# Kernel tuning notes

Hardware: AMD Instinct MI355X
Metric: run time of the kernel (lower is better)

The kernel has to match this reference:

```python
import jax, jax.numpy as jnp
import numpy as np

L = 8          # context_length
P = 196        # patches_per_frame
PT = 16        # patches_per_tactile_frame
N_EMBD = 768
N_HEAD = 12
BATCH = 4
T = (L + 1) + L * PT + L * P  # 1705


def build_mask(L, P, Pt):
    # image-query block rows (L*P rows)
    mi = np.zeros((L * P, L * P))
    a1 = np.zeros((L * P, L + 1))
    t1 = np.zeros((L * P, L * Pt))
    for i in range(L):
        mi[i * P:(i + 1) * P, :(i + 1) * P] = 1
        a1[i * P:(i + 2) * P, :i + 2] = 1
        t1[i * P:(i + 1) * P, :(i + 1) * Pt] = 1
    m1 = np.concatenate([a1, t1, mi], axis=1)
    # tactile-query block rows (L*Pt rows)
    a2 = np.zeros((L * Pt, L + 1))
    t2 = np.zeros((L * Pt, L * Pt))
    i2 = np.zeros((L * Pt, L * P))
    for i in range(L):
        a2[i * Pt:(i + 2) * Pt, :i + 2] = 1
        t2[i * Pt:(i + 1) * Pt, :(i + 1) * Pt] = 1
        i2[i * Pt:(i + 1) * Pt, :(i + 1) * P] = 1
    m2 = np.concatenate([a2, t2, i2], axis=1)
    # action-query rows (L+1 rows)
    a3 = np.zeros((L + 1, L + 1))
    t3 = np.zeros((L + 1, L * Pt))
    i3 = np.zeros((L + 1, L * P))
    for i in range(L + 1):
        a3[i:i + 2, :i + 2] = 1
        t3[i:i + 1, :(i + 1) * Pt] = 1
        i3[i:i + 1, :(i + 1) * P] = 1
    m3 = np.concatenate([a3, t3, i3], axis=1)
    return np.concatenate([m3, m2, m1], axis=0).astype(bool)


def setup_inputs() -> dict:
    key = jax.random.key(0)
    k1, k2, k3 = jax.random.split(key, 3)
    x = jax.random.normal(k1, (BATCH, T, N_EMBD), dtype=jnp.float32)
    W_attn = jax.random.normal(k2, (N_EMBD, 3 * N_EMBD), dtype=jnp.float32) * 0.02
    W_proj = jax.random.normal(k3, (N_EMBD, N_EMBD), dtype=jnp.float32) * 0.02
    mask = jnp.asarray(build_mask(L, P, PT))
    return {"x": x, "W_attn": W_attn, "W_proj": W_proj, "mask": mask, "n_head": N_HEAD}


def reference(x, W_attn, W_proj, mask, n_head):
    B, Tq, C = x.shape
    hd = C // n_head
    qkv = x @ W_attn                      # [B, T, 3C]
    q, k, v = jnp.split(qkv, 3, axis=-1)
    # [B, H, T, hd]
    q = q.reshape(B, Tq, n_head, hd).transpose(0, 2, 1, 3)
    k = k.reshape(B, Tq, n_head, hd).transpose(0, 2, 1, 3)
    v = v.reshape(B, Tq, n_head, hd).transpose(0, 2, 1, 3)
    scores = jnp.einsum("bhqd,bhkd->bhqk", q, k) / jnp.sqrt(jnp.float32(hd))
    scores = jnp.where(mask[None, None, :, :], scores, jnp.float32(-1e9))
    probs = jax.nn.softmax(scores, axis=-1)
    y = jnp.einsum("bhqk,bhkd->bhqd", probs, v)
    y = y.transpose(0, 2, 1, 3).reshape(B, Tq, C)
    return y @ W_proj
```

## Files before the change

### kernel.cpp

```cpp
#include <hip/hip_runtime.h>
#include <hip/hip_bf16.h>

typedef __attribute__((ext_vector_type(8))) short short8;
typedef __attribute__((ext_vector_type(4))) float f32x4;

#define MFMA16(a,b,c) __builtin_amdgcn_mfma_f32_16x16x32_bf16((a),(b),(c),0,0,0)

#define WAITVM3_BAR() asm volatile("s_waitcnt vmcnt(3)\n\ts_barrier" ::: "memory")
#define WAITVM0_BAR() asm volatile("s_waitcnt vmcnt(0)\n\ts_barrier" ::: "memory")
#define LG0_BAR()     asm volatile("s_waitcnt lgkmcnt(0)\n\ts_barrier" ::: "memory")

constexpr int Tt = 1705;
constexpr int Tp = 1792;
constexpr int NKT_ALL = 28;
constexpr int NH = 12, HD = 64, Bb = 4, C_ = 768;
constexpr int M_  = Bb * Tt;
constexpr int Mp  = 6912;
constexpr int NQT = 14;
constexpr int NCH = 4;
constexpr float QSCALE = 0.18033688011116016f;

static_assert(Mp % 256 == 0 && (3 * C_) % 256 == 0, "256-tile grid");

__device__ __forceinline__ void gl16(const void* g, void* l) {
  __builtin_amdgcn_global_load_lds((const __attribute__((address_space(1))) void*)g,
                                   (__attribute__((address_space(3))) void*)l, 16, 0, 0);
}

__device__ __forceinline__ float ex2(float x) {
  float r; asm("v_exp_f32 %0, %1" : "=v"(r) : "v"(x)); return r;
}

__device__ __forceinline__ int frame_of(int t) {
  return t < 9 ? t : (t < 137 ? ((t - 9) >> 4) : ((t - 137) / 196));
}

__device__ __forceinline__ int lim16(int a) {
  if (a >= Tt) return 0;
  int bnd = min(a + 15, Tt - 1);
  int fmax = (a == 0) ? 8 : frame_of(min(bnd, a < 137 ? 136 : bnd));
  return (fmax >= 8) ? Tt : 137 + (fmax + 1) * 196;
}

__global__ __launch_bounds__(256) void k_conv_x(const float* __restrict__ x,
                                                __hip_bfloat16* __restrict__ xb) {
  int i = blockIdx.x * 256 + threadIdx.x;
  if (i >= Mp * C_ / 4) return;
  float4 v = make_float4(0.f, 0.f, 0.f, 0.f);
  if (i * 4 < M_ * C_) v = ((const float4*)x)[i];
  __hip_bfloat16 o0 = __float2bfloat16(v.x), o1 = __float2bfloat16(v.y),
                 o2 = __float2bfloat16(v.z), o3 = __float2bfloat16(v.w);
  ushort4 u = make_ushort4(*(unsigned short*)&o0, *(unsigned short*)&o1,
                           *(unsigned short*)&o2, *(unsigned short*)&o3);
  ((ushort4*)xb)[i] = u;
}

__global__ __launch_bounds__(256) void k_transpose_w(const float* __restrict__ src,
                                                     __hip_bfloat16* __restrict__ dst,
                                                     int K, int N) {
  __shared__ float tile[32][33];
  int kb = blockIdx.x * 32, nb = blockIdx.y * 32;
  int tx = threadIdx.x & 31, ty = threadIdx.x >> 5;
  for (int i = 0; i < 4; i++)
    tile[ty + i * 8][tx] = src[(size_t)(kb + ty + i * 8) * N + nb + tx];
  __syncthreads();
  for (int i = 0; i < 4; i++)
    dst[(size_t)(nb + ty + i * 8) * K + kb + tx] = __float2bfloat16(tile[tx][ty + i * 8]);
}

__global__ __launch_bounds__(512) void k_gemm_qkv(const __hip_bfloat16* __restrict__ xb,
                                                  const __hip_bfloat16* __restrict__ wat,
                                                  __hip_bfloat16* __restrict__ q,
                                                  __hip_bfloat16* __restrict__ kpk,
                                                  __hip_bfloat16* __restrict__ vpk) {
  __shared__ __hip_bfloat16 As[2][256 * 32], Bs[2][256 * 32];
  const int tid = threadIdx.x;
  const int lane = tid & 63, w = tid >> 6;
  const int wr = w >> 2, wc = w & 3;
  const int l16 = lane & 15, grp = lane >> 4;
  const int m0 = blockIdx.x * 256, n0 = blockIdx.y * 256;
  constexpr int NT = C_ / 32;

  auto stage_pass = [&](int t, int bb, int p) {
    int idx = p * 512 + tid;
    int row = idx >> 2;
    int c8 = (idx & 3) ^ ((row >> 1) & 3);
    int k0 = t * 32;
    gl16(xb  + (size_t)(m0 + row) * C_ + k0 + c8 * 8, &As[bb][idx * 8]);
    gl16(wat + (size_t)(n0 + row) * C_ + k0 + c8 * 8, &Bs[bb][idx * 8]);
  };

  f32x4 acc[8][4];
  for (int i = 0; i < 8; i++)
    for (int j = 0; j < 4; j++) { f32x4 z = {0.f,0.f,0.f,0.f}; acc[i][j] = z; }

  stage_pass(0, 0, 0);
  stage_pass(0, 0, 1);
  WAITVM0_BAR();

  for (int t = 0; t < NT; t++) {
    const int cur = t & 1, nxt = cur ^ 1;
    const __hip_bfloat16* Ac = As[cur];
    const __hip_bfloat16* Bc = Bs[cur];
    short8 bfr[4], afr[4];
    if (t + 1 < NT) stage_pass(t + 1, nxt, 0);
    for (int nj = 0; nj < 4; nj++) {
      int row = wc * 64 + nj * 16 + l16;
      bfr[nj] = *(const short8*)(Bc + row * 32 + ((grp ^ ((row >> 1) & 3)) * 8));
    }
    for (int mi = 0; mi < 4; mi++) {
      int row = wr * 128 + mi * 16 + l16;
      afr[mi] = *(const short8*)(Ac + row * 32 + ((grp ^ ((row >> 1) & 3)) * 8));
    }
    __builtin_amdgcn_s_setprio(1);
    for (int mi = 0; mi < 4; mi++)
      for (int nj = 0; nj < 4; nj++)
        acc[mi][nj] = MFMA16(afr[mi], bfr[nj], acc[mi][nj]);
    __builtin_amdgcn_s_setprio(0);
    if (t + 1 < NT) stage_pass(t + 1, nxt, 1);
    for (int mi = 0; mi < 4; mi++) {
      int row = wr * 128 + 64 + mi * 16 + l16;
      afr[mi] = *(const short8*)(Ac + row * 32 + ((grp ^ ((row >> 1) & 3)) * 8));
    }
    __builtin_amdgcn_s_setprio(1);
    for (int mi = 0; mi < 4; mi++)
      for (int nj = 0; nj < 4; nj++)
        acc[4 + mi][nj] = MFMA16(afr[mi], bfr[nj], acc[4 + mi][nj]);
    __builtin_amdgcn_s_setprio(0);
    WAITVM0_BAR();
  }

  const int which = n0 / C_;
  const int c0 = n0 - which * C_ + wc * 64;
  for (int mi = 0; mi < 8; mi++)
    for (int r = 0; r < 4; r++) {
      int m = m0 + wr * 128 + mi * 16 + grp * 4 + r;
      if (m >= M_) continue;
      int b = m / Tt, t = m - b * Tt;
      for (int nj = 0; nj < 4; nj++) {
        int c = c0 + nj * 16 + l16;
        int h = c >> 6, d = c & 63;
        float val = acc[mi][nj][r];
        int bh = b * NH + h;
        if (which == 0) {
          q[((size_t)bh * Tp + t) * HD + d] = __float2bfloat16(val * QSCALE);
        } else if (which == 1) {
          int kt = t >> 6, jj = (t >> 4) & 3, mm = t & 15;
          int half = d >> 5, gg = (d >> 3) & 3, ss = d & 7;
          kpk[(((size_t)bh * NKT_ALL + kt) * 8 + jj * 2 + half) * 512 +
              (gg * 16 + mm) * 8 + ss] = __float2bfloat16(val);
        } else {
          int kt = t >> 6, kb2 = (t >> 5) & 1, k32 = t & 31;
          int gg = (k32 >> 2) & 3, ss = (k32 & 3) + ((k32 >> 4) & 1) * 4;
          int jt = d >> 4, mm = d & 15;
          vpk[(((size_t)bh * NKT_ALL + kt) * 8 + jt * 2 + kb2) * 512 +
              (gg * 16 + mm) * 8 + ss] = __float2bfloat16(val);
        }
      }
    }
}

__global__ __launch_bounds__(256) void k_gemm_proj64(const __hip_bfloat16* __restrict__ A,
                                                     const __hip_bfloat16* __restrict__ Bt,
                                                     float* __restrict__ out) {
  __shared__ __hip_bfloat16 As0[64 * 32], Bs0[128 * 32];
  __shared__ __hip_bfloat16 As1[64 * 32], Bs1[128 * 32];
  const int tid = threadIdx.x;
  const int lane = tid & 63, w = tid >> 6;
  const int l16 = lane & 15, grp = lane >> 4;
  const int m0 = blockIdx.x * 64, n0 = blockIdx.y * 128;
  f32x4 acc[8];
  for (int j = 0; j < 8; j++) { f32x4 z = {0.f,0.f,0.f,0.f}; acc[j] = z; }

  auto stage = [&](int k0, __hip_bfloat16* As, __hip_bfloat16* Bs) {
    int row = tid >> 2;
    int c8 = (tid & 3) ^ ((row >> 1) & 3);
    gl16(A + (size_t)(m0 + row) * C_ + k0 + c8 * 8, As + tid * 8);
    for (int rr = 0; rr < 2; rr++) {
      int idx = rr * 256 + tid;
      int brow = idx >> 2;
      int bc8 = (idx & 3) ^ ((brow >> 1) & 3);
      gl16(Bt + (size_t)(n0 + brow) * C_ + k0 + bc8 * 8, Bs + idx * 8);
    }
  };
  auto comp = [&](const __hip_bfloat16* As, const __hip_bfloat16* Bs) {
    int arow = w * 16 + l16;
    short8 a = *(const short8*)(As + arow * 32 + ((grp ^ ((arow >> 1) & 3)) * 8));
    for (int j = 0; j < 8; j++) {
      int brow = j * 16 + l16;
      short8 b = *(const short8*)(Bs + brow * 32 + ((grp ^ ((brow >> 1) & 3)) * 8));
      acc[j] = MFMA16(a, b, acc[j]);
    }
  };

  constexpr int NP = C_ >> 6;
  stage(0, As0, Bs0);
  for (int p = 0; p < NP; p++) {
    int k0 = p << 6;
    stage(k0 + 32, As1, Bs1);
    WAITVM3_BAR();
    comp(As0, Bs0);
    LG0_BAR();
    if (p + 1 < NP) {
      stage(k0 + 64, As0, Bs0);
      WAITVM3_BAR();
    } else {
      WAITVM0_BAR();
    }
    comp(As1, Bs1);
    LG0_BAR();
  }

  for (int r = 0; r < 4; r++) {
    int m = m0 + w * 16 + grp * 4 + r;
    if (m >= M_) continue;
    for (int j = 0; j < 8; j++)
      out[(size_t)m * C_ + n0 + j * 16 + l16] = acc[j][r];
  }
}

union S8u { short8 v; struct { unsigned long long lo, hi; } q; unsigned u[4]; };

__device__ __forceinline__ unsigned pack2bf(float a, float b) {
  union { __hip_bfloat162 h; unsigned u; } cv;
  cv.h = __float22bfloat162_rn(make_float2(a, b));
  return cv.u;
}

__global__ __launch_bounds__(256, 2) void k_attn(const __hip_bfloat16* __restrict__ q,
                                                 const __hip_bfloat16* __restrict__ kpk,
                                                 const __hip_bfloat16* __restrict__ vpk,
                                                 __hip_bfloat16* __restrict__ Opart,
                                                 float* __restrict__ lpart) {
  const int tid = threadIdx.x, lane = tid & 63, w = tid >> 6;
  const int l16 = lane & 15, grp = lane >> 4;
  const int id = blockIdx.x;
  const int xslot = id & 7, rr_ = id >> 3;
  const int bh = xslot + 8 * (rr_ / 56);
  const int cq = rr_ % 56;
  const int qt = cq >> 2, ch = cq & (NCH - 1);
  const int t0q = qt * 128;
  const __hip_bfloat16* qb = q + (size_t)bh * Tp * HD;

  int lim[2], Cmn[2], Ath[2], Bth[2], Cth[2];
  for (int g = 0; g < 2; g++) {
    int a = t0q + w * 32 + g * 16;
    lim[g] = lim16(a);
    int fqmn, fql;
    if (a >= Tt) { fqmn = 8; fql = 8; }
    else {
      int bnd = min(a + 15, Tt - 1);
      fqmn = min(frame_of(a), frame_of(bnd));
      int t = a + l16;
      fql = (t >= Tt) ? 8 : frame_of(t);
    }
    Cmn[g] = min(137 + 196 * (fqmn + 1), Tt);
    Ath[g] = fql + 2;
    Bth[g] = 9 + 16 * (fql + 1);
    Cth[g] = min(137 + 196 * (fql + 1), Tt);
  }
  int limw = max(lim[0], lim[1]);
  int nktw = (limw + 63) >> 6;
  int k0t = (ch * nktw) >> 2;
  int k1t = ((ch + 1) * nktw) >> 2;

  short8 qa[2][2];
  for (int g = 0; g < 2; g++) {
    const __hip_bfloat16* qr = qb + (size_t)(t0q + w * 32 + g * 16 + l16) * HD + grp * 8;
    qa[g][0] = *(const short8*)(qr);
    qa[g][1] = *(const short8*)(qr + 32);
  }
  f32x4 o[2][4];
  for (int g = 0; g < 2; g++)
    for (int jt = 0; jt < 4; jt++) { f32x4 z = {0.f,0.f,0.f,0.f}; o[g][jt] = z; }
  f32x4 ps[2];
  { f32x4 z = {0.f,0.f,0.f,0.f}; ps[0] = z; ps[1] = z; }

  const short8* kbase = (const short8*)(kpk + (size_t)bh * NKT_ALL * 4096);
  const short8* vbase = (const short8*)(vpk + (size_t)bh * NKT_ALL * 4096);

  for (int kt = k0t; kt < k1t; kt++) {
    const int t0k = kt * 64;
    const short8* kp = kbase + (size_t)kt * 512;
    const short8* vp = vbase + (size_t)kt * 512;
    short8 kf[4][2], vf[4][2];
    for (int j = 0; j < 4; j++)
      for (int hh = 0; hh < 2; hh++) kf[j][hh] = kp[(j * 2 + hh) * 64 + lane];
    for (int jt = 0; jt < 4; jt++)
      for (int kb2 = 0; kb2 < 2; kb2++) vf[jt][kb2] = vp[(jt * 2 + kb2) * 64 + lane];

    f32x4 s[2][4];
    for (int j = 0; j < 4; j++) {
      f32x4 z = {0.f,0.f,0.f,0.f};
      s[0][j] = MFMA16(kf[j][0], qa[0][0], z);
      s[0][j] = MFMA16(kf[j][1], qa[0][1], s[0][j]);
      s[1][j] = MFMA16(kf[j][0], qa[1][0], z);
      s[1][j] = MFMA16(kf[j][1], qa[1][1], s[1][j]);
    }

    bool act0 = t0k < lim[0], act1 = t0k < lim[1];
    bool fullk = (t0k + 64 <= Tt);
    S8u pf[2][2];
    for (int g = 0; g < 2; g++) {
      bool act = g == 0 ? act0 : act1;
      if (!act) continue;
      bool needm = !(fullk && (t0k >= 192 ? (t0k + 64) <= Cmn[g] : Cmn[g] >= Tt));
      if (needm) {
        for (int j = 0; j < 4; j++)
          for (int r = 0; r < 4; r++) {
            int key = t0k + j * 16 + grp * 4 + r;
            int thr = key < 9 ? Ath[g] : (key < 137 ? Bth[g] : Cth[g]);
            if (key >= thr) s[g][j][r] = -1e30f;
          }
      }
      f32x4 p[4];
      for (int j = 0; j < 4; j++)
        for (int r = 0; r < 4; r++) p[j][r] = ex2(s[g][j][r]);
      ps[g] += (p[0] + p[1]) + (p[2] + p[3]);
      pf[g][0].u[0] = pack2bf(p[0][0], p[0][1]);
      pf[g][0].u[1] = pack2bf(p[0][2], p[0][3]);
      pf[g][0].u[2] = pack2bf(p[1][0], p[1][1]);
      pf[g][0].u[3] = pack2bf(p[1][2], p[1][3]);
      pf[g][1].u[0] = pack2bf(p[2][0], p[2][1]);
      pf[g][1].u[1] = pack2bf(p[2][2], p[2][3]);
      pf[g][1].u[2] = pack2bf(p[3][0], p[3][1]);
      pf[g][1].u[3] = pack2bf(p[3][2], p[3][3]);
    }

    for (int jt = 0; jt < 4; jt++)
      for (int kb2 = 0; kb2 < 2; kb2++) {
        if (act0) o[0][jt] = MFMA16(vf[jt][kb2], pf[0][kb2].v, o[0][jt]);
        if (act1) o[1][jt] = MFMA16(vf[jt][kb2], pf[1][kb2].v, o[1][jt]);
      }
  }

  float lr[2];
  for (int g = 0; g < 2; g++) {
    float sum = (ps[g][0] + ps[g][1]) + (ps[g][2] + ps[g][3]);
    sum += __shfl_xor(sum, 16);
    sum += __shfl_xor(sum, 32);
    lr[g] = sum;
  }

  const int blk = bh * (NQT * NCH) + cq;
  __hip_bfloat16* op = Opart + (size_t)blk * (128 * 64);
  for (int g = 0; g < 2; g++) {
    int row = w * 32 + g * 16 + l16;
    for (int jt = 0; jt < 4; jt++) {
      unsigned p01 = pack2bf(o[g][jt][0], o[g][jt][1]);
      unsigned p23 = pack2bf(o[g][jt][2], o[g][jt][3]);
      ushort4 u;
      u.x = p01 & 0xffff; u.y = p01 >> 16; u.z = p23 & 0xffff; u.w = p23 >> 16;
      *(ushort4*)(op + row * 64 + jt * 16 + grp * 4) = u;
    }
    if (grp == 0) lpart[(size_t)blk * 128 + w * 32 + g * 16 + l16] = lr[g];
  }
}

__global__ __launch_bounds__(256) void k_combine(const __hip_bfloat16* __restrict__ Opart,
                                                 const float* __restrict__ lpart,
                                                 __hip_bfloat16* __restrict__ y) {
  const int tid = threadIdx.x;
  const int qt = blockIdx.x, bh = blockIdx.y;
  const int b = bh / NH, h = bh - b * NH;
  const int t0q = qt * 128;
  const int blk0 = bh * (NQT * NCH) + qt * NCH;
  __shared__ float ls[128];
  if (tid < 128) {
    float s = 0.f;
    for (int c = 0; c < NCH; c++) s += lpart[(size_t)(blk0 + c) * 128 + tid];
    ls[tid] = (s > 0.f) ? 1.0f / s : 0.f;
  }
  __syncthreads();
  for (int it = 0; it < 4; it++) {
    int e8 = it * 256 + tid;
    int e = e8 * 8;
    int row = e >> 6, d = e & 63;
    int t = t0q + row;
    if (t >= Tt) continue;
    float acc[8] = {0,0,0,0,0,0,0,0};
    for (int c = 0; c < NCH; c++) {
      short8 vv = *(const short8*)(Opart + (size_t)(blk0 + c) * (128 * 64) + e);
      for (int i = 0; i < 8; i++) {
        union { unsigned u; float f; } cv;
        cv.u = ((unsigned)(unsigned short)vv[i]) << 16;
        acc[i] += cv.f;
      }
    }
    float rinv = ls[row];
    short8 outv;
    for (int i = 0; i < 8; i += 2) {
      unsigned p = pack2bf(acc[i] * rinv, acc[i + 1] * rinv);
      outv[i] = (short)(p & 0xffff);
      outv[i + 1] = (short)(p >> 16);
    }
    *(short8*)(y + (size_t)(b * Tt + t) * C_ + h * 64 + d) = outv;
  }
}

extern "C" void kernel_launch(void* const* d_in, const int* in_sizes, int n_in,
                              void* d_out, int out_size, void* d_ws, size_t ws_size,
                              hipStream_t stream) {
  const float* x  = (const float*)d_in[0];
  const float* Wa = (const float*)d_in[1];
  const float* Wp = (const float*)d_in[2];
  float* out = (float*)d_out;

  char* ws = (char*)d_ws;
  size_t off = 0;
  auto alloc = [&](size_t bytes) { size_t r = off; off += (bytes + 255) & ~(size_t)255; return r; };
  __hip_bfloat16* xb  = (__hip_bfloat16*)(ws + alloc((size_t)Mp * C_ * 2));
  __hip_bfloat16* wat = (__hip_bfloat16*)(ws + alloc((size_t)3 * C_ * C_ * 2));
  __hip_bfloat16* wpt = (__hip_bfloat16*)(ws + alloc((size_t)C_ * C_ * 2));
  __hip_bfloat16* qb  = (__hip_bfloat16*)(ws + alloc((size_t)Bb * NH * Tp * HD * 2));
  __hip_bfloat16* kpk = (__hip_bfloat16*)(ws + alloc((size_t)Bb * NH * NKT_ALL * 4096 * 2));
  __hip_bfloat16* vpk = (__hip_bfloat16*)(ws + alloc((size_t)Bb * NH * NKT_ALL * 4096 * 2));
  __hip_bfloat16* yb  = (__hip_bfloat16*)(ws + alloc((size_t)Mp * C_ * 2));
  __hip_bfloat16* Opart = (__hip_bfloat16*)(ws + alloc((size_t)Bb * NH * NQT * NCH * 128 * 64 * 2));
  float*          lpart = (float*)(ws + alloc((size_t)Bb * NH * NQT * NCH * 128 * 4));

  k_conv_x<<<(Mp * C_ / 4 + 255) / 256, 256, 0, stream>>>(x, xb);
  k_transpose_w<<<dim3(C_ / 32, 3 * C_ / 32), 256, 0, stream>>>(Wa, wat, C_, 3 * C_);
  k_transpose_w<<<dim3(C_ / 32, C_ / 32), 256, 0, stream>>>(Wp, wpt, C_, C_);
  k_gemm_qkv<<<dim3(Mp / 256, 3 * C_ / 256), 512, 0, stream>>>(xb, wat, qb, kpk, vpk);
  k_attn<<<dim3(Bb * NH * NQT * NCH), 256, 0, stream>>>(qb, kpk, vpk, Opart, lpart);
  k_combine<<<dim3(NQT, Bb * NH), 256, 0, stream>>>(Opart, lpart, yb);
  k_gemm_proj64<<<dim3(Mp / 64, C_ / 128), 256, 0, stream>>>(yb, wpt, out);
}
```

Measured before the change: 218.6 us.

## Deepen QKV and projection GEMM pipelines to four-stage LDS ring buffers

Both the QKV GEMM and the output-projection GEMM now use a four-buffer LDS ring with three K-tiles of global_load_lds in flight, instead of double buffering. Partial vmcnt waits replace the full vmcnt(0) drain on each iteration, so global loads overlap more MFMA work. The QKV kernel's LDS use doubles to 128 KB, which may lower occupancy. The projection kernel also gains s_setprio around its MFMAs.

```diff
diff --git a/kernel.cpp b/kernel.cpp
--- a/kernel.cpp
+++ b/kernel.cpp
@@ -6,9 +6,8 @@
 
 #define MFMA16(a,b,c) __builtin_amdgcn_mfma_f32_16x16x32_bf16((a),(b),(c),0,0,0)
 
-#define WAITVM3_BAR() asm volatile("s_waitcnt vmcnt(3)\n\ts_barrier" ::: "memory")
-#define WAITVM0_BAR() asm volatile("s_waitcnt vmcnt(0)\n\ts_barrier" ::: "memory")
-#define LG0_BAR()     asm volatile("s_waitcnt lgkmcnt(0)\n\ts_barrier" ::: "memory")
+#define WAITVM(N) asm volatile("s_waitcnt vmcnt(" #N ")" ::: "memory")
+#define BAR()     asm volatile("s_barrier" ::: "memory")
 
 constexpr int Tt = 1705;
 constexpr int Tp = 1792;
@@ -73,7 +72,7 @@
                                                   __hip_bfloat16* __restrict__ q,
                                                   __hip_bfloat16* __restrict__ kpk,
                                                   __hip_bfloat16* __restrict__ vpk) {
-  __shared__ __hip_bfloat16 As[2][256 * 32], Bs[2][256 * 32];
+  __shared__ __hip_bfloat16 As[4][256 * 32], Bs[4][256 * 32];
   const int tid = threadIdx.x;
   const int lane = tid & 63, w = tid >> 6;
   const int wr = w >> 2, wc = w & 3;
@@ -81,29 +80,34 @@
   const int m0 = blockIdx.x * 256, n0 = blockIdx.y * 256;
   constexpr int NT = C_ / 32;
 
-  auto stage_pass = [&](int t, int bb, int p) {
-    int idx = p * 512 + tid;
-    int row = idx >> 2;
-    int c8 = (idx & 3) ^ ((row >> 1) & 3);
+  auto stage = [&](int t, int bb) {
     int k0 = t * 32;
-    gl16(xb  + (size_t)(m0 + row) * C_ + k0 + c8 * 8, &As[bb][idx * 8]);
-    gl16(wat + (size_t)(n0 + row) * C_ + k0 + c8 * 8, &Bs[bb][idx * 8]);
+    for (int p = 0; p < 2; p++) {
+      int idx = p * 512 + tid;
+      int row = idx >> 2;
+      int c8 = (idx & 3) ^ ((row >> 1) & 3);
+      gl16(xb  + (size_t)(m0 + row) * C_ + k0 + c8 * 8, &As[bb][idx * 8]);
+      gl16(wat + (size_t)(n0 + row) * C_ + k0 + c8 * 8, &Bs[bb][idx * 8]);
+    }
   };
 
   f32x4 acc[8][4];
   for (int i = 0; i < 8; i++)
     for (int j = 0; j < 4; j++) { f32x4 z = {0.f,0.f,0.f,0.f}; acc[i][j] = z; }
 
-  stage_pass(0, 0, 0);
-  stage_pass(0, 0, 1);
-  WAITVM0_BAR();
+  stage(0, 0); stage(1, 1); stage(2, 2);
 
   for (int t = 0; t < NT; t++) {
-    const int cur = t & 1, nxt = cur ^ 1;
-    const __hip_bfloat16* Ac = As[cur];
-    const __hip_bfloat16* Bc = Bs[cur];
+    if (t + 3 < NT) stage(t + 3, (t + 3) & 3);
+    int rem = NT - 1 - t;
+    if (rem >= 3)      WAITVM(12);
+    else if (rem == 2) WAITVM(8);
+    else if (rem == 1) WAITVM(4);
+    else               WAITVM(0);
+    BAR();
+    const __hip_bfloat16* Ac = As[t & 3];
+    const __hip_bfloat16* Bc = Bs[t & 3];
     short8 bfr[4], afr[4];
-    if (t + 1 < NT) stage_pass(t + 1, nxt, 0);
     for (int nj = 0; nj < 4; nj++) {
       int row = wc * 64 + nj * 16 + l16;
       bfr[nj] = *(const short8*)(Bc + row * 32 + ((grp ^ ((row >> 1) & 3)) * 8));
@@ -117,7 +121,6 @@
       for (int nj = 0; nj < 4; nj++)
         acc[mi][nj] = MFMA16(afr[mi], bfr[nj], acc[mi][nj]);
     __builtin_amdgcn_s_setprio(0);
-    if (t + 1 < NT) stage_pass(t + 1, nxt, 1);
     for (int mi = 0; mi < 4; mi++) {
       int row = wr * 128 + 64 + mi * 16 + l16;
       afr[mi] = *(const short8*)(Ac + row * 32 + ((grp ^ ((row >> 1) & 3)) * 8));
@@ -127,7 +130,7 @@
       for (int nj = 0; nj < 4; nj++)
         acc[4 + mi][nj] = MFMA16(afr[mi], bfr[nj], acc[4 + mi][nj]);
     __builtin_amdgcn_s_setprio(0);
-    WAITVM0_BAR();
+    BAR();
   }
 
   const int which = n0 / C_;
@@ -163,8 +166,7 @@
 __global__ __launch_bounds__(256) void k_gemm_proj64(const __hip_bfloat16* __restrict__ A,
                                                      const __hip_bfloat16* __restrict__ Bt,
                                                      float* __restrict__ out) {
-  __shared__ __hip_bfloat16 As0[64 * 32], Bs0[128 * 32];
-  __shared__ __hip_bfloat16 As1[64 * 32], Bs1[128 * 32];
+  __shared__ __hip_bfloat16 As[4][64 * 32], Bs[4][128 * 32];
   const int tid = threadIdx.x;
   const int lane = tid & 63, w = tid >> 6;
   const int l16 = lane & 15, grp = lane >> 4;
@@ -172,43 +174,42 @@
   f32x4 acc[8];
   for (int j = 0; j < 8; j++) { f32x4 z = {0.f,0.f,0.f,0.f}; acc[j] = z; }
 
-  auto stage = [&](int k0, __hip_bfloat16* As, __hip_bfloat16* Bs) {
+  auto stage = [&](int t, int bb) {
+    int k0 = t * 32;
     int row = tid >> 2;
     int c8 = (tid & 3) ^ ((row >> 1) & 3);
-    gl16(A + (size_t)(m0 + row) * C_ + k0 + c8 * 8, As + tid * 8);
+    gl16(A + (size_t)(m0 + row) * C_ + k0 + c8 * 8, &As[bb][tid * 8]);
     for (int rr = 0; rr < 2; rr++) {
       int idx = rr * 256 + tid;
       int brow = idx >> 2;
       int bc8 = (idx & 3) ^ ((brow >> 1) & 3);
-      gl16(Bt + (size_t)(n0 + brow) * C_ + k0 + bc8 * 8, Bs + idx * 8);
+      gl16(Bt + (size_t)(n0 + brow) * C_ + k0 + bc8 * 8, &Bs[bb][idx * 8]);
     }
   };
-  auto comp = [&](const __hip_bfloat16* As, const __hip_bfloat16* Bs) {
+
+  constexpr int NT = C_ / 32;
+  stage(0, 0); stage(1, 1); stage(2, 2);
+
+  for (int t = 0; t < NT; t++) {
+    if (t + 3 < NT) stage(t + 3, (t + 3) & 3);
+    int rem = NT - 1 - t;
+    if (rem >= 3)      WAITVM(9);
+    else if (rem == 2) WAITVM(6);
+    else if (rem == 1) WAITVM(3);
+    else               WAITVM(0);
+    BAR();
+    const __hip_bfloat16* Ac = As[t & 3];
+    const __hip_bfloat16* Bc = Bs[t & 3];
     int arow = w * 16 + l16;
-    short8 a = *(const short8*)(As + arow * 32 + ((grp ^ ((arow >> 1) & 3)) * 8));
+    short8 a = *(const short8*)(Ac + arow * 32 + ((grp ^ ((arow >> 1) & 3)) * 8));
+    __builtin_amdgcn_s_setprio(1);
     for (int j = 0; j < 8; j++) {
       int brow = j * 16 + l16;
-      short8 b = *(const short8*)(Bs + brow * 32 + ((grp ^ ((brow >> 1) & 3)) * 8));
+      short8 b = *(const short8*)(Bc + brow * 32 + ((grp ^ ((brow >> 1) & 3)) * 8));
       acc[j] = MFMA16(a, b, acc[j]);
     }
-  };
-
-  constexpr int NP = C_ >> 6;
-  stage(0, As0, Bs0);
-  for (int p = 0; p < NP; p++) {
-    int k0 = p << 6;
-    stage(k0 + 32, As1, Bs1);
-    WAITVM3_BAR();
-    comp(As0, Bs0);
-    LG0_BAR();
-    if (p + 1 < NP) {
-      stage(k0 + 64, As0, Bs0);
-      WAITVM3_BAR();
-    } else {
-      WAITVM0_BAR();
-    }
-    comp(As1, Bs1);
-    LG0_BAR();
+    __builtin_amdgcn_s_setprio(0);
+    BAR();
   }
 
   for (int r = 0; r < 4; r++) {
```

After: 221.3 us. About the same (+1.2%).
